# Kernel tuning notes

Measured on AMD Instinct MI355X. Metric: run time of the kernel, lower is better.

The kernel has to match this reference:

```python
import jax, jax.numpy as jnp
import numpy as np

D_MODEL = 1024
N_HEAD = 16
D_HEAD = 64


def setup_inputs() -> dict:
    key = jax.random.key(0)
    k1, k2, k3 = jax.random.split(key, 3)
    B, T = 2, 2048
    x = jax.random.normal(k1, (B, T, D_MODEL), dtype=jnp.float32)
    # Linear weights (scaled like typical init to keep softmax numerics sane)
    w_attn = jax.random.normal(k2, (D_MODEL, 3 * D_MODEL), dtype=jnp.float32) * (1.0 / np.sqrt(D_MODEL))
    w_proj = jax.random.normal(k3, (D_MODEL, D_MODEL), dtype=jnp.float32) * (1.0 / np.sqrt(D_MODEL))
    return {"x": x, "w_attn": w_attn, "w_proj": w_proj}


def reference(x, w_attn, w_proj):
    B, T, C = x.shape
    # c_attn: fused qkv projection (use_bias=False)
    qkv = jnp.einsum('btc,cf->btf', x, w_attn)  # [B, T, 3C]
    q, k, v = jnp.split(qkv, 3, axis=-1)
    q = q.reshape(B, T, N_HEAD, D_HEAD)
    k = k.reshape(B, T, N_HEAD, D_HEAD)
    v = v.reshape(B, T, N_HEAD, D_HEAD)
    # scaled QK^T with causal mask (cache=None training path)
    att = jnp.einsum('bqhd,bkhd->bhqk', q, k) * (1.0 / jnp.sqrt(jnp.float32(D_HEAD)))
    causal = jnp.tril(jnp.ones((T, T), dtype=bool))  # [T, T]
    att = jnp.where(causal[None, None, :, :], att, -jnp.inf)
    att = jax.nn.softmax(att, axis=-1)
    # dropout is a no-op (deterministic / p=0)
    y = jnp.einsum('bhqk,bkhd->bqhd', att, v).reshape(B, T, C)
    y = jnp.einsum('btc,cd->btd', y, w_proj)
    return y
```

## Files before the change

### kernel.cpp

```cpp
#include <hip/hip_runtime.h>
#include <hip/hip_bf16.h>


typedef __attribute__((ext_vector_type(8))) __bf16 bf16x8;
typedef __attribute__((ext_vector_type(4))) float  floatx4;
typedef __attribute__((ext_vector_type(4))) float  fvec4;
typedef __attribute__((ext_vector_type(4))) short  short4v;

#define MFMA16(a, b, c) __builtin_amdgcn_mfma_f32_16x16x32_bf16(a, b, c, 0, 0, 0)

using as1v = const __attribute__((address_space(1))) void;
using as3v = __attribute__((address_space(3))) void;
__device__ __forceinline__ void async16(const void* g, void* l) {
  __builtin_amdgcn_global_load_lds((as1v*)g, (as3v*)l, 16, 0, 0);
}

__device__ inline void store_out(float* p, float v) { *p = v; }
__device__ inline void store_out(__hip_bfloat16* p, float v) { *p = __float2bfloat16(v); }

__global__ __launch_bounds__(256) void cast_bf16_kernel(const float* __restrict__ in,
                                                        __hip_bfloat16* __restrict__ out,
                                                        int n) {
  int i = (blockIdx.x * 256 + threadIdx.x) * 4;
  if (i >= n) return;
  fvec4 v = *(const fvec4*)(in + i);
  union { short4v s; __hip_bfloat16 h[4]; } u;
#pragma unroll
  for (int j = 0; j < 4; ++j) u.h[j] = __float2bfloat16(v[j]);
  *(short4v*)((short*)out + i) = u.s;
}

__global__ __launch_bounds__(256) void transpose_cast_kernel(const float* __restrict__ in,
                                                             __hip_bfloat16* __restrict__ out,
                                                             int rows, int cols) {
  __shared__ float tile[32][33];
  const int tx = threadIdx.x, ty = threadIdx.y;
  const int c0 = blockIdx.x * 32, r0 = blockIdx.y * 32;
#pragma unroll
  for (int i = 0; i < 32; i += 8)
    tile[ty + i][tx] = in[(long)(r0 + ty + i) * cols + c0 + tx];
  __syncthreads();
#pragma unroll
  for (int i = 0; i < 32; i += 8)
    out[(long)(c0 + ty + i) * rows + r0 + tx] = __float2bfloat16(tile[tx][ty + i]);
}

__global__ __launch_bounds__(256) void vt_kernel(const __hip_bfloat16* __restrict__ qkv,
                                                 __hip_bfloat16* __restrict__ vt) {
  __shared__ __align__(16) __hip_bfloat16 tile[64 * 64];
  const int tid = threadIdx.x;
  const int tt0 = blockIdx.x * 64, h = blockIdx.y, b = blockIdx.z;
  const long bh = (long)b * 16 + h;
#pragma unroll
  for (int it = 0; it < 2; ++it) {
    const int c = it * 256 + tid;
    const int row = c >> 3, cg = c & 7;
    const int pg = cg ^ ((row >> 3) & 7);
    *(bf16x8*)(tile + row * 64 + pg * 8) =
        *(const bf16x8*)(qkv + ((long)b * 2048 + tt0 + row) * 3072 + 2048 + h * 64 + cg * 8);
  }
  __syncthreads();
#pragma unroll
  for (int it = 0; it < 2; ++it) {
    const int c = it * 256 + tid;
    const int dr = c >> 3, tg = c & 7;
    union { bf16x8 v; __hip_bfloat16 e[8]; } u;
    const int pg = (dr >> 3) ^ tg;
#pragma unroll
    for (int j = 0; j < 8; ++j)
      u.e[j] = tile[(tg * 8 + j) * 64 + pg * 8 + (dr & 7)];
    *(bf16x8*)(vt + (bh * 64 + dr) * 2048 + tt0 + tg * 8) = u.v;
  }
}

template <typename OutT>
__global__ __launch_bounds__(256) void gemm_bt_kernel(const __hip_bfloat16* __restrict__ A,
                                                      const __hip_bfloat16* __restrict__ Bt,
                                                      OutT* __restrict__ C,
                                                      int M, int N, int K) {
  __shared__ __align__(16) __hip_bfloat16 As[2][128 * 32];
  __shared__ __align__(16) __hip_bfloat16 Bs[2][128 * 32];
  const int tid = threadIdx.x;
  const int lane = tid & 63, wv = tid >> 6;
  const int l15 = lane & 15, quad = lane >> 4;
  const int wm = wv >> 1, wn = wv & 1;
  const long m0 = (long)blockIdx.y * 128, n0 = (long)blockIdx.x * 128;
  floatx4 acc[4][4] = {};
  const int nk = K >> 5;

  auto issue = [&](int kt, int p) {
    const int k0 = kt << 5;
#pragma unroll
    for (int it = 0; it < 2; ++it) {
      const int c = it * 256 + tid;
      const int row = c >> 2;
      const int lcg = (c & 3) ^ ((row >> 1) & 3);
      const int ldsoff = c * 16;
      async16(A + (m0 + row) * K + k0 + lcg * 8, (char*)&As[p][0] + ldsoff);
      async16(Bt + (n0 + row) * K + k0 + lcg * 8, (char*)&Bs[p][0] + ldsoff);
    }
  };

  issue(0, 0);
  for (int kt = 0; kt < nk; ++kt) {
    const int p = kt & 1;
    __syncthreads();
    if (kt + 1 < nk) issue(kt + 1, p ^ 1);
    bf16x8 af[4], bfr[4];
#pragma unroll
    for (int t = 0; t < 4; ++t) {
      const int ar = wm * 64 + t * 16 + l15;
      const int br = wn * 64 + t * 16 + l15;
      af[t]  = *(const bf16x8*)(&As[p][ar * 32 + (quad ^ ((ar >> 1) & 3)) * 8]);
      bfr[t] = *(const bf16x8*)(&Bs[p][br * 32 + (quad ^ ((br >> 1) & 3)) * 8]);
    }
#pragma unroll
    for (int mt = 0; mt < 4; ++mt)
#pragma unroll
      for (int nt = 0; nt < 4; ++nt)
        acc[mt][nt] = MFMA16(af[mt], bfr[nt], acc[mt][nt]);
  }
#pragma unroll
  for (int mt = 0; mt < 4; ++mt)
#pragma unroll
    for (int nt = 0; nt < 4; ++nt)
#pragma unroll
      for (int r = 0; r < 4; ++r) {
        const long row = m0 + wm * 64 + mt * 16 + quad * 4 + r;
        const long col = n0 + wn * 64 + nt * 16 + l15;
        store_out(C + row * N + col, acc[mt][nt][r]);
      }
}

__global__ __launch_bounds__(256) void attn_kernel(const __hip_bfloat16* __restrict__ qkv,
                                                   const __hip_bfloat16* __restrict__ vtg,
                                                   __hip_bfloat16* __restrict__ y) {
  __shared__ __align__(16) __hip_bfloat16 Ks[2][64 * 64];
  __shared__ __align__(16) __hip_bfloat16 Vt[2][64 * 64];
  __shared__ __align__(16) __hip_bfloat16 Ps[2 * 4 * 16 * 72];
  const int tid = threadIdx.x;
  const int lane = tid & 63, wv = tid >> 6;
  const int l15 = lane & 15, quad = lane >> 4;
  const int pt = blockIdx.x, h = blockIdx.y, b = blockIdx.z;
  const int qtA = pt, qtB = 31 - pt;
  const int q0A = qtA * 64, q0B = qtB * 64;
  const long bh = (long)b * 16 + h;
  const long RS = 3072;
  const float SC = 0.18033688011112042f;

  auto issue = [&](int kt, int p) {
    const int kb = kt * 64;
#pragma unroll
    for (int it = 0; it < 2; ++it) {
      const int c = it * 256 + tid;
      const int row = c >> 3;
      const int cg = (c & 7) ^ (row & 7);
      const int ldsoff = c * 16;
      async16(qkv + ((long)b * 2048 + kb + row) * RS + 1024 + h * 64 + cg * 8,
              (char*)&Ks[p][0] + ldsoff);
      async16(vtg + (bh * 64 + row) * 2048 + kb + cg * 8, (char*)&Vt[p][0] + ldsoff);
    }
  };

  bf16x8 aqA0, aqA1, aqB0, aqB1;
  {
    const __hip_bfloat16* qpA = qkv + ((long)b * 2048 + q0A + wv * 16 + l15) * RS + h * 64 + quad * 8;
    aqA0 = *(const bf16x8*)qpA;
    aqA1 = *(const bf16x8*)(qpA + 32);
    const __hip_bfloat16* qpB = qkv + ((long)b * 2048 + q0B + wv * 16 + l15) * RS + h * 64 + quad * 8;
    aqB0 = *(const bf16x8*)qpB;
    aqB1 = *(const bf16x8*)(qpB + 32);
  }
  union { bf16x8 v; __hip_bfloat16 e[8]; } uo;
#pragma unroll
  for (int j = 0; j < 8; ++j) uo.e[j] = __float2bfloat16(1.0f);
  const bf16x8 ones = uo.v;

  floatx4 oA[4] = {}, oB[4] = {}, o4A = {}, o4B = {};
  __hip_bfloat16* PsA = Ps + wv * 1152;
  __hip_bfloat16* PsB = Ps + 4608 + wv * 1152;

  issue(0, 0);
  for (int kt = 0; kt <= qtB; ++kt) {
    const int p = kt & 1;
    const int kb = kt * 64;
    const bool actA = (kt <= qtA);
    __syncthreads();
    if (kt < qtB) issue(kt + 1, p ^ 1);

    bf16x8 kf[4][2], vf[4][2];
#pragma unroll
    for (int nt = 0; nt < 4; ++nt) {
      const int row = nt * 16 + l15;
      const int s0 = (quad ^ (row & 7)) * 8, s1 = ((quad + 4) ^ (row & 7)) * 8;
      kf[nt][0] = *(const bf16x8*)(&Ks[p][row * 64 + s0]);
      kf[nt][1] = *(const bf16x8*)(&Ks[p][row * 64 + s1]);
      vf[nt][0] = *(const bf16x8*)(&Vt[p][row * 64 + s0]);
      vf[nt][1] = *(const bf16x8*)(&Vt[p][row * 64 + s1]);
    }

    floatx4 sB[4] = {}, sA[4] = {};
#pragma unroll
    for (int nt = 0; nt < 4; ++nt) {
      sB[nt] = MFMA16(aqB0, kf[nt][0], sB[nt]);
      sB[nt] = MFMA16(aqB1, kf[nt][1], sB[nt]);
    }
    if (actA) {
#pragma unroll
      for (int nt = 0; nt < 4; ++nt) {
        sA[nt] = MFMA16(aqA0, kf[nt][0], sA[nt]);
        sA[nt] = MFMA16(aqA1, kf[nt][1], sA[nt]);
      }
    }

    auto do_sm = [&](floatx4* s, __hip_bfloat16* PsX, bool diag, int q0X) {
#pragma unroll
      for (int nt = 0; nt < 4; ++nt)
#pragma unroll
        for (int r = 0; r < 4; ++r) {
          float pv = exp2f(s[nt][r] * SC);
          if (diag && (kb + nt * 16 + l15 > q0X + wv * 16 + quad * 4 + r)) pv = 0.f;
          PsX[(quad * 4 + r) * 72 + nt * 16 + l15] = __float2bfloat16(pv);
        }
    };
    do_sm(sB, PsB, kt == qtB, q0B);
    if (actA) do_sm(sA, PsA, kt == qtA, q0A);

    {
      const __hip_bfloat16* pp = PsB + l15 * 72 + quad * 8;
      const bf16x8 p0 = *(const bf16x8*)pp, p1 = *(const bf16x8*)(pp + 32);
#pragma unroll
      for (int nt = 0; nt < 4; ++nt) {
        oB[nt] = MFMA16(p0, vf[nt][0], oB[nt]);
        oB[nt] = MFMA16(p1, vf[nt][1], oB[nt]);
      }
      o4B = MFMA16(p0, ones, o4B);
      o4B = MFMA16(p1, ones, o4B);
    }
    if (actA) {
      const __hip_bfloat16* pp = PsA + l15 * 72 + quad * 8;
      const bf16x8 p0 = *(const bf16x8*)pp, p1 = *(const bf16x8*)(pp + 32);
#pragma unroll
      for (int nt = 0; nt < 4; ++nt) {
        oA[nt] = MFMA16(p0, vf[nt][0], oA[nt]);
        oA[nt] = MFMA16(p1, vf[nt][1], oA[nt]);
      }
      o4A = MFMA16(p0, ones, o4A);
      o4A = MFMA16(p1, ones, o4A);
    }
  }

#pragma unroll
  for (int r = 0; r < 4; ++r) {
    const float invA = 1.0f / o4A[r];
    const float invB = 1.0f / o4B[r];
    const long tA = (long)b * 2048 + q0A + wv * 16 + quad * 4 + r;
    const long tB = (long)b * 2048 + q0B + wv * 16 + quad * 4 + r;
#pragma unroll
    for (int nt = 0; nt < 4; ++nt) {
      y[tA * 1024 + h * 64 + nt * 16 + l15] = __float2bfloat16(oA[nt][r] * invA);
      y[tB * 1024 + h * 64 + nt * 16 + l15] = __float2bfloat16(oB[nt][r] * invB);
    }
  }
}

extern "C" void kernel_launch(void* const* d_in, const int* in_sizes, int n_in,
                              void* d_out, int out_size, void* d_ws, size_t ws_size,
                              hipStream_t stream) {
  const float* x      = (const float*)d_in[0];
  const float* w_attn = (const float*)d_in[1];
  const float* w_proj = (const float*)d_in[2];
  float* out = (float*)d_out;
  char* ws = (char*)d_ws;
  __hip_bfloat16* xb   = (__hip_bfloat16*)(ws);
  __hip_bfloat16* wat  = (__hip_bfloat16*)(ws + 8388608);
  __hip_bfloat16* qkvb = (__hip_bfloat16*)(ws + 16777216);
  __hip_bfloat16* wpt  = (__hip_bfloat16*)(ws + 41943040);
  __hip_bfloat16* vtg  = xb;
  __hip_bfloat16* yb   = wat;

  cast_bf16_kernel<<<4096, 256, 0, stream>>>(x, xb, 4194304);
  transpose_cast_kernel<<<dim3(96, 32), dim3(32, 8), 0, stream>>>(w_attn, wat, 1024, 3072);
  transpose_cast_kernel<<<dim3(32, 32), dim3(32, 8), 0, stream>>>(w_proj, wpt, 1024, 1024);
  gemm_bt_kernel<__hip_bfloat16><<<dim3(24, 32), 256, 0, stream>>>(xb, wat, qkvb, 4096, 3072, 1024);
  vt_kernel<<<dim3(32, 16, 2), 256, 0, stream>>>(qkvb, vtg);
  attn_kernel<<<dim3(16, 16, 2), 256, 0, stream>>>(qkvb, vtg, yb);
  gemm_bt_kernel<float><<<dim3(8, 32), 256, 0, stream>>>(yb, wpt, out, 4096, 1024, 1024);
}
```

Measured before the change: 201.3 us.

## Merge prep kernels, fold softmax scale into QKV GEMM, split attention tiles, narrow proj GEMM

Merges the x cast and the two weight transpose-casts into one prep kernel launch. The softmax scale is now applied to the Q columns in the QKV GEMM epilogue, so attention no longer multiplies by it per element. Attention drops the paired-tile load balancing (tiles qt and 31-qt per block) in favour of one query tile per block with twice the grid, peels the masked diagonal step, and uses an XOR-swizzled P buffer in LDS instead of a padded one. The output projection uses a new 128x64-tile GEMM to launch more blocks. The trade-off is causal work imbalance across blocks and extra K/V loads, since each block now streams its own K/V.

```diff
diff --git a/kernel.cpp b/kernel.cpp
--- a/kernel.cpp
+++ b/kernel.cpp
@@ -18,24 +18,35 @@
 __device__ inline void store_out(float* p, float v) { *p = v; }
 __device__ inline void store_out(__hip_bfloat16* p, float v) { *p = __float2bfloat16(v); }
 
-__global__ __launch_bounds__(256) void cast_bf16_kernel(const float* __restrict__ in,
-                                                        __hip_bfloat16* __restrict__ out,
-                                                        int n) {
-  int i = (blockIdx.x * 256 + threadIdx.x) * 4;
-  if (i >= n) return;
-  fvec4 v = *(const fvec4*)(in + i);
-  union { short4v s; __hip_bfloat16 h[4]; } u;
-#pragma unroll
-  for (int j = 0; j < 4; ++j) u.h[j] = __float2bfloat16(v[j]);
-  *(short4v*)((short*)out + i) = u.s;
-}
-
-__global__ __launch_bounds__(256) void transpose_cast_kernel(const float* __restrict__ in,
-                                                             __hip_bfloat16* __restrict__ out,
-                                                             int rows, int cols) {
+__global__ __launch_bounds__(256) void prep_kernel(const float* __restrict__ x,
+                                                   const float* __restrict__ w_attn,
+                                                   const float* __restrict__ w_proj,
+                                                   __hip_bfloat16* __restrict__ xb,
+                                                   __hip_bfloat16* __restrict__ wat,
+                                                   __hip_bfloat16* __restrict__ wpt) {
   __shared__ float tile[32][33];
-  const int tx = threadIdx.x, ty = threadIdx.y;
-  const int c0 = blockIdx.x * 32, r0 = blockIdx.y * 32;
+  const int bid = blockIdx.x, tid = threadIdx.x;
+  if (bid < 4096) {
+    const int i = (bid * 256 + tid) * 4;
+    fvec4 v = *(const fvec4*)(x + i);
+    union { short4v s; __hip_bfloat16 h[4]; } u;
+#pragma unroll
+    for (int j = 0; j < 4; ++j) u.h[j] = __float2bfloat16(v[j]);
+    *(short4v*)((short*)xb + i) = u.s;
+    return;
+  }
+  const float* in;
+  __hip_bfloat16* out;
+  int rows, cols, bx, by;
+  if (bid < 4096 + 3072) {
+    const int b2 = bid - 4096;
+    in = w_attn; out = wat; rows = 1024; cols = 3072; bx = b2 % 96; by = b2 / 96;
+  } else {
+    const int b2 = bid - 7168;
+    in = w_proj; out = wpt; rows = 1024; cols = 1024; bx = b2 % 32; by = b2 / 32;
+  }
+  const int tx = tid & 31, ty = tid >> 5;
+  const int c0 = bx * 32, r0 = by * 32;
 #pragma unroll
   for (int i = 0; i < 32; i += 8)
     tile[ty + i][tx] = in[(long)(r0 + ty + i) * cols + c0 + tx];
@@ -77,7 +88,8 @@
 __global__ __launch_bounds__(256) void gemm_bt_kernel(const __hip_bfloat16* __restrict__ A,
                                                       const __hip_bfloat16* __restrict__ Bt,
                                                       OutT* __restrict__ C,
-                                                      int M, int N, int K) {
+                                                      int M, int N, int K,
+                                                      float qscale, int qlim) {
   __shared__ __align__(16) __hip_bfloat16 As[2][128 * 32];
   __shared__ __align__(16) __hip_bfloat16 Bs[2][128 * 32];
   const int tid = threadIdx.x;
@@ -95,9 +107,8 @@
       const int c = it * 256 + tid;
       const int row = c >> 2;
       const int lcg = (c & 3) ^ ((row >> 1) & 3);
-      const int ldsoff = c * 16;
-      async16(A + (m0 + row) * K + k0 + lcg * 8, (char*)&As[p][0] + ldsoff);
-      async16(Bt + (n0 + row) * K + k0 + lcg * 8, (char*)&Bs[p][0] + ldsoff);
+      async16(A + (m0 + row) * K + k0 + lcg * 8, (char*)&As[p][0] + c * 16);
+      async16(Bt + (n0 + row) * K + k0 + lcg * 8, (char*)&Bs[p][0] + c * 16);
     }
   };
 
@@ -128,6 +139,74 @@
       for (int r = 0; r < 4; ++r) {
         const long row = m0 + wm * 64 + mt * 16 + quad * 4 + r;
         const long col = n0 + wn * 64 + nt * 16 + l15;
+        float v = acc[mt][nt][r];
+        if ((int)col < qlim) v *= qscale;
+        store_out(C + row * N + col, v);
+      }
+}
+
+template <typename OutT>
+__global__ __launch_bounds__(256) void gemm_bt64_kernel(const __hip_bfloat16* __restrict__ A,
+                                                        const __hip_bfloat16* __restrict__ Bt,
+                                                        OutT* __restrict__ C,
+                                                        int M, int N, int K) {
+  __shared__ __align__(16) __hip_bfloat16 As[2][128 * 32];
+  __shared__ __align__(16) __hip_bfloat16 Bs[2][64 * 32];
+  const int tid = threadIdx.x;
+  const int lane = tid & 63, wv = tid >> 6;
+  const int l15 = lane & 15, quad = lane >> 4;
+  const int wm = wv >> 1, wn = wv & 1;
+  const long m0 = (long)blockIdx.y * 128, n0 = (long)blockIdx.x * 64;
+  floatx4 acc[4][2] = {};
+  const int nk = K >> 5;
+
+  auto issue = [&](int kt, int p) {
+    const int k0 = kt << 5;
+#pragma unroll
+    for (int it = 0; it < 2; ++it) {
+      const int c = it * 256 + tid;
+      const int row = c >> 2;
+      const int lcg = (c & 3) ^ ((row >> 1) & 3);
+      async16(A + (m0 + row) * K + k0 + lcg * 8, (char*)&As[p][0] + c * 16);
+    }
+    {
+      const int c = tid;
+      const int row = c >> 2;
+      const int lcg = (c & 3) ^ ((row >> 1) & 3);
+      async16(Bt + (n0 + row) * K + k0 + lcg * 8, (char*)&Bs[p][0] + c * 16);
+    }
+  };
+
+  issue(0, 0);
+  for (int kt = 0; kt < nk; ++kt) {
+    const int p = kt & 1;
+    __syncthreads();
+    if (kt + 1 < nk) issue(kt + 1, p ^ 1);
+    bf16x8 af[4], bfr[2];
+#pragma unroll
+    for (int t = 0; t < 4; ++t) {
+      const int ar = wm * 64 + t * 16 + l15;
+      af[t] = *(const bf16x8*)(&As[p][ar * 32 + (quad ^ ((ar >> 1) & 3)) * 8]);
+    }
+#pragma unroll
+    for (int t = 0; t < 2; ++t) {
+      const int br = wn * 32 + t * 16 + l15;
+      bfr[t] = *(const bf16x8*)(&Bs[p][br * 32 + (quad ^ ((br >> 1) & 3)) * 8]);
+    }
+#pragma unroll
+    for (int mt = 0; mt < 4; ++mt)
+#pragma unroll
+      for (int nt = 0; nt < 2; ++nt)
+        acc[mt][nt] = MFMA16(af[mt], bfr[nt], acc[mt][nt]);
+  }
+#pragma unroll
+  for (int mt = 0; mt < 4; ++mt)
+#pragma unroll
+    for (int nt = 0; nt < 2; ++nt)
+#pragma unroll
+      for (int r = 0; r < 4; ++r) {
+        const long row = m0 + wm * 64 + mt * 16 + quad * 4 + r;
+        const long col = n0 + wn * 32 + nt * 16 + l15;
         store_out(C + row * N + col, acc[mt][nt][r]);
       }
 }
@@ -137,16 +216,14 @@
                                                    __hip_bfloat16* __restrict__ y) {
   __shared__ __align__(16) __hip_bfloat16 Ks[2][64 * 64];
   __shared__ __align__(16) __hip_bfloat16 Vt[2][64 * 64];
-  __shared__ __align__(16) __hip_bfloat16 Ps[2 * 4 * 16 * 72];
+  __shared__ __align__(16) __hip_bfloat16 Ps[4 * 16 * 64];
   const int tid = threadIdx.x;
   const int lane = tid & 63, wv = tid >> 6;
   const int l15 = lane & 15, quad = lane >> 4;
-  const int pt = blockIdx.x, h = blockIdx.y, b = blockIdx.z;
-  const int qtA = pt, qtB = 31 - pt;
-  const int q0A = qtA * 64, q0B = qtB * 64;
+  const int qt = blockIdx.x, h = blockIdx.y, b = blockIdx.z;
+  const int q0 = qt * 64;
   const long bh = (long)b * 16 + h;
   const long RS = 3072;
-  const float SC = 0.18033688011112042f;
 
   auto issue = [&](int kt, int p) {
     const int kb = kt * 64;
@@ -155,39 +232,28 @@
       const int c = it * 256 + tid;
       const int row = c >> 3;
       const int cg = (c & 7) ^ (row & 7);
-      const int ldsoff = c * 16;
       async16(qkv + ((long)b * 2048 + kb + row) * RS + 1024 + h * 64 + cg * 8,
-              (char*)&Ks[p][0] + ldsoff);
-      async16(vtg + (bh * 64 + row) * 2048 + kb + cg * 8, (char*)&Vt[p][0] + ldsoff);
+              (char*)&Ks[p][0] + c * 16);
+      async16(vtg + (bh * 64 + row) * 2048 + kb + cg * 8, (char*)&Vt[p][0] + c * 16);
     }
   };
 
-  bf16x8 aqA0, aqA1, aqB0, aqB1;
+  bf16x8 aq0, aq1;
   {
-    const __hip_bfloat16* qpA = qkv + ((long)b * 2048 + q0A + wv * 16 + l15) * RS + h * 64 + quad * 8;
-    aqA0 = *(const bf16x8*)qpA;
-    aqA1 = *(const bf16x8*)(qpA + 32);
-    const __hip_bfloat16* qpB = qkv + ((long)b * 2048 + q0B + wv * 16 + l15) * RS + h * 64 + quad * 8;
-    aqB0 = *(const bf16x8*)qpB;
-    aqB1 = *(const bf16x8*)(qpB + 32);
+    const __hip_bfloat16* qp = qkv + ((long)b * 2048 + q0 + wv * 16 + l15) * RS + h * 64 + quad * 8;
+    aq0 = *(const bf16x8*)qp;
+    aq1 = *(const bf16x8*)(qp + 32);
   }
   union { bf16x8 v; __hip_bfloat16 e[8]; } uo;
 #pragma unroll
   for (int j = 0; j < 8; ++j) uo.e[j] = __float2bfloat16(1.0f);
   const bf16x8 ones = uo.v;
 
-  floatx4 oA[4] = {}, oB[4] = {}, o4A = {}, o4B = {};
-  __hip_bfloat16* PsA = Ps + wv * 1152;
-  __hip_bfloat16* PsB = Ps + 4608 + wv * 1152;
-
-  issue(0, 0);
-  for (int kt = 0; kt <= qtB; ++kt) {
-    const int p = kt & 1;
+  floatx4 o[4] = {}, o4 = {};
+  __hip_bfloat16* Psw = Ps + wv * 1024;
+
+  auto compute = [&](int kt, int p, bool mask) {
     const int kb = kt * 64;
-    const bool actA = (kt <= qtA);
-    __syncthreads();
-    if (kt < qtB) issue(kt + 1, p ^ 1);
-
     bf16x8 kf[4][2], vf[4][2];
 #pragma unroll
     for (int nt = 0; nt < 4; ++nt) {
@@ -198,69 +264,55 @@
       vf[nt][0] = *(const bf16x8*)(&Vt[p][row * 64 + s0]);
       vf[nt][1] = *(const bf16x8*)(&Vt[p][row * 64 + s1]);
     }
-
-    floatx4 sB[4] = {}, sA[4] = {};
+    floatx4 s[4] = {};
 #pragma unroll
     for (int nt = 0; nt < 4; ++nt) {
-      sB[nt] = MFMA16(aqB0, kf[nt][0], sB[nt]);
-      sB[nt] = MFMA16(aqB1, kf[nt][1], sB[nt]);
-    }
-    if (actA) {
-#pragma unroll
-      for (int nt = 0; nt < 4; ++nt) {
-        sA[nt] = MFMA16(aqA0, kf[nt][0], sA[nt]);
-        sA[nt] = MFMA16(aqA1, kf[nt][1], sA[nt]);
+      s[nt] = MFMA16(aq0, kf[nt][0], s[nt]);
+      s[nt] = MFMA16(aq1, kf[nt][1], s[nt]);
+    }
+#pragma unroll
+    for (int nt = 0; nt < 4; ++nt)
+#pragma unroll
+      for (int r = 0; r < 4; ++r) {
+        float pv = exp2f(s[nt][r]);
+        if (mask && (kb + nt * 16 + l15 > q0 + wv * 16 + quad * 4 + r)) pv = 0.f;
+        const int row = quad * 4 + r;
+        const int pg = (nt * 2 + (l15 >> 3)) ^ (row & 7);
+        Psw[row * 64 + pg * 8 + (l15 & 7)] = __float2bfloat16(pv);
       }
-    }
-
-    auto do_sm = [&](floatx4* s, __hip_bfloat16* PsX, bool diag, int q0X) {
-#pragma unroll
-      for (int nt = 0; nt < 4; ++nt)
-#pragma unroll
-        for (int r = 0; r < 4; ++r) {
-          float pv = exp2f(s[nt][r] * SC);
-          if (diag && (kb + nt * 16 + l15 > q0X + wv * 16 + quad * 4 + r)) pv = 0.f;
-          PsX[(quad * 4 + r) * 72 + nt * 16 + l15] = __float2bfloat16(pv);
-        }
-    };
-    do_sm(sB, PsB, kt == qtB, q0B);
-    if (actA) do_sm(sA, PsA, kt == qtA, q0A);
-
-    {
-      const __hip_bfloat16* pp = PsB + l15 * 72 + quad * 8;
-      const bf16x8 p0 = *(const bf16x8*)pp, p1 = *(const bf16x8*)(pp + 32);
-#pragma unroll
-      for (int nt = 0; nt < 4; ++nt) {
-        oB[nt] = MFMA16(p0, vf[nt][0], oB[nt]);
-        oB[nt] = MFMA16(p1, vf[nt][1], oB[nt]);
-      }
-      o4B = MFMA16(p0, ones, o4B);
-      o4B = MFMA16(p1, ones, o4B);
-    }
-    if (actA) {
-      const __hip_bfloat16* pp = PsA + l15 * 72 + quad * 8;
-      const bf16x8 p0 = *(const bf16x8*)pp, p1 = *(const bf16x8*)(pp + 32);
-#pragma unroll
-      for (int nt = 0; nt < 4; ++nt) {
-        oA[nt] = MFMA16(p0, vf[nt][0], oA[nt]);
-        oA[nt] = MFMA16(p1, vf[nt][1], oA[nt]);
-      }
-      o4A = MFMA16(p0, ones, o4A);
-      o4A = MFMA16(p1, ones, o4A);
-    }
+    const int m7 = l15 & 7;
+    const __hip_bfloat16* pb = Psw + l15 * 64;
+    const bf16x8 p0 = *(const bf16x8*)(pb + (quad ^ m7) * 8);
+    const bf16x8 p1 = *(const bf16x8*)(pb + ((quad + 4) ^ m7) * 8);
+#pragma unroll
+    for (int nt = 0; nt < 4; ++nt) {
+      o[nt] = MFMA16(p0, vf[nt][0], o[nt]);
+      o[nt] = MFMA16(p1, vf[nt][1], o[nt]);
+    }
+    o4 = MFMA16(p0, ones, o4);
+    o4 = MFMA16(p1, ones, o4);
+  };
+
+  issue(0, 0);
+  for (int kt = 0; kt < qt; ++kt) {
+    const int p = kt & 1;
+    __syncthreads();
+    issue(kt + 1, p ^ 1);
+    compute(kt, p, false);
+  }
+  {
+    const int p = qt & 1;
+    __syncthreads();
+    compute(qt, p, true);
   }
 
 #pragma unroll
   for (int r = 0; r < 4; ++r) {
-    const float invA = 1.0f / o4A[r];
-    const float invB = 1.0f / o4B[r];
-    const long tA = (long)b * 2048 + q0A + wv * 16 + quad * 4 + r;
-    const long tB = (long)b * 2048 + q0B + wv * 16 + quad * 4 + r;
-#pragma unroll
-    for (int nt = 0; nt < 4; ++nt) {
-      y[tA * 1024 + h * 64 + nt * 16 + l15] = __float2bfloat16(oA[nt][r] * invA);
-      y[tB * 1024 + h * 64 + nt * 16 + l15] = __float2bfloat16(oB[nt][r] * invB);
-    }
+    const float inv = 1.0f / o4[r];
+    const long t = (long)b * 2048 + q0 + wv * 16 + quad * 4 + r;
+#pragma unroll
+    for (int nt = 0; nt < 4; ++nt)
+      y[t * 1024 + h * 64 + nt * 16 + l15] = __float2bfloat16(o[nt][r] * inv);
   }
 }
 
@@ -278,12 +330,11 @@
   __hip_bfloat16* wpt  = (__hip_bfloat16*)(ws + 41943040);
   __hip_bfloat16* vtg  = xb;
   __hip_bfloat16* yb   = wat;
-
-  cast_bf16_kernel<<<4096, 256, 0, stream>>>(x, xb, 4194304);
-  transpose_cast_kernel<<<dim3(96, 32), dim3(32, 8), 0, stream>>>(w_attn, wat, 1024, 3072);
-  transpose_cast_kernel<<<dim3(32, 32), dim3(32, 8), 0, stream>>>(w_proj, wpt, 1024, 1024);
-  gemm_bt_kernel<__hip_bfloat16><<<dim3(24, 32), 256, 0, stream>>>(xb, wat, qkvb, 4096, 3072, 1024);
+  const float SC = 0.18033688011112042f;
+
+  prep_kernel<<<8192, 256, 0, stream>>>(x, w_attn, w_proj, xb, wat, wpt);
+  gemm_bt_kernel<__hip_bfloat16><<<dim3(24, 32), 256, 0, stream>>>(xb, wat, qkvb, 4096, 3072, 1024, SC, 1024);
   vt_kernel<<<dim3(32, 16, 2), 256, 0, stream>>>(qkvb, vtg);
-  attn_kernel<<<dim3(16, 16, 2), 256, 0, stream>>>(qkvb, vtg, yb);
-  gemm_bt_kernel<float><<<dim3(8, 32), 256, 0, stream>>>(yb, wpt, out, 4096, 1024, 1024);
-}
+  attn_kernel<<<dim3(32, 16, 2), 256, 0, stream>>>(qkvb, vtg, yb);
+  gemm_bt64_kernel<float><<<dim3(16, 32), 256, 0, stream>>>(yb, wpt, out, 4096, 1024, 1024);
+}
```

After: 234.1 us. +16.3%, slower.
